# Optimization experiments

Hardware: AMD Instinct MI355X
Metric: run time of the kernel (lower is better)

Reference implementation:

```python
import jax, jax.numpy as jnp
import numpy as np

B, CIN, H, W = 32, 512, 64, 64
HID, A, C = 256, 9, 20
M = 65536


def setup_inputs() -> dict:
    key = jax.random.key(0)
    k = jax.random.split(key, 7)
    N = B * A * H * W
    features = jax.random.normal(k[0], (B, CIN, H, W), jnp.float32)
    W1 = jax.random.normal(k[1], (HID, CIN), jnp.float32) * 0.02
    b1 = jnp.zeros((HID,), jnp.float32)
    W2 = jax.random.normal(k[2], (5 * A + C, HID), jnp.float32) * 0.02
    b2 = jnp.zeros((5 * A + C,), jnp.float32)
    pos_anchor_idx = jax.random.randint(k[3], (M,), 0, N, jnp.int64 if jax.config.read('jax_enable_x64') else jnp.int32)
    neg_anchor_idx = jax.random.randint(k[4], (M,), 0, N, jnp.int64 if jax.config.read('jax_enable_x64') else jnp.int32)
    return {"features": features, "W1": W1, "b1": b1, "W2": W2, "b2": b2,
            "pos_anchor_idx": pos_anchor_idx, "neg_anchor_idx": neg_anchor_idx}


def reference(features, W1, b1, W2, b2, pos_anchor_idx, neg_anchor_idx):
    Bb, Cin, Hh, Ww = features.shape
    # 1x1 convs are channel GEMMs
    h = jnp.einsum('bchw,oc->bohw', features, W1) + b1[None, :, None, None]
    h = jax.nn.leaky_relu(h, 0.01)  # Dropout2d identity at inference
    out = jnp.einsum('bchw,oc->bohw', h, W2) + b2[None, :, None, None]
    class_scores = out[:, 5 * A:, :, :]                      # (B, C, H, W)
    anchor = out[:, :5 * A, :, :].reshape(Bb, A, 5, Hh, Ww)   # (B, A, 5, H, W)
    conf = jax.nn.sigmoid(anchor[:, :, 0:1])                  # (B, A, 1, H, W)
    off = anchor[:, :, 1:]                                    # (B, A, 4, H, W)
    off = jnp.concatenate([jax.nn.sigmoid(off[:, :, :2]) - 0.5, off[:, :, 2:]], axis=2)
    # extraction: flat layout is b*A*H*W + a*H*W + h*W + w (permute 0,1,3,4,2)
    off_flat = off.transpose(0, 1, 3, 4, 2).reshape(-1, 4)
    conf_flat = conf.transpose(0, 1, 3, 4, 2).reshape(-1, 1)
    offsets = off_flat[pos_anchor_idx]                        # (M, 4)
    conf_out = jnp.concatenate([conf_flat[pos_anchor_idx], conf_flat[neg_anchor_idx]], axis=0)  # (2M, 1)
    # class scores: expand over A is a pure broadcast, so index by (b, spatial) directly
    b_idx = pos_anchor_idx // (A * Hh * Ww)
    sp = pos_anchor_idx % (Hh * Ww)
    cls_flat = class_scores.transpose(0, 2, 3, 1).reshape(Bb * Hh * Ww, -1)
    class_out = cls_flat[b_idx * (Hh * Ww) + sp]              # (M, C)
    return conf_out, offsets, class_out
```

## Files before the change

### kernel.cpp

```cpp
#include <hip/hip_runtime.h>
#include <hip/hip_bf16.h>

typedef __attribute__((ext_vector_type(8)))  __bf16 bf16x8;
typedef __attribute__((ext_vector_type(4)))  __bf16 bf16x4;
typedef __attribute__((ext_vector_type(16))) float  f32x16;
typedef __attribute__((ext_vector_type(4)))  float  f32x4;

#define B_    32
#define CIN   512
#define HID   256
#define HW    4096
#define NA    9
#define NCH   65
#define NPADC 96
#define BN    128
#define M_    65536
#define NTOT  (B_*NA*HW)


static __device__ __forceinline__ float sigf(float v) {
    return 1.f / (1.f + __expf(-v));
}

__global__ void prep_weights(const float* __restrict__ W1, const float* __restrict__ W2,
                             unsigned short* __restrict__ W1bt, unsigned short* __restrict__ W2p) {
    int i = blockIdx.x * 256 + threadIdx.x;
    if (i < 16*256*32) {
        int kt = i >> 13, o = (i >> 5) & 255, kk = i & 31;
        __bf16 h = (__bf16)W1[o*CIN + kt*32 + kk];
        W1bt[i] = __builtin_bit_cast(unsigned short, h);
    } else {
        int j = i - 16*256*32;
        if (j < NPADC*HID) {
            int o = j >> 8, c = j & 255;
            float v = (o < NCH) ? W2[o*HID + c] : 0.f;
            __bf16 h = (__bf16)v;
            W2p[j] = __builtin_bit_cast(unsigned short, h);
        }
    }
}

__launch_bounds__(256, 2)
__global__ void fused_mlp(const float* __restrict__ feat,
                          const float* __restrict__ b1,
                          const float* __restrict__ b2,
                          const unsigned short* __restrict__ W1bt,
                          const unsigned short* __restrict__ W2p,
                          float* __restrict__ conf_d,
                          unsigned short* __restrict__ off_w,
                          unsigned short* __restrict__ cls_w) {
    __shared__ __align__(16) unsigned char smem[65536];
    unsigned short* As = (unsigned short*)smem;
    unsigned short* Bs = (unsigned short*)(smem + 20480);

    const int tid  = threadIdx.x;
    const int w    = tid >> 6;
    const int lane = tid & 63;
    const int lr   = lane & 31;
    const int lh   = lane >> 5;
    const int bidx = blockIdx.x >> 5;
    const int hw0  = (blockIdx.x & 31) * BN;

    const float* fb = feat + (size_t)bidx * CIN * HW + hw0;

    const int sA  = tid;
    const int sB  = tid & 127;
    const int kgB = tid >> 7;

    f32x16 acc[2][4];
#pragma unroll
    for (int m = 0; m < 2; ++m)
#pragma unroll
        for (int n = 0; n < 4; ++n) acc[m][n] = (f32x16)0.f;

    bf16x8 pa[4];
    float  pb[16];

    auto loadA = [&](int kt) {
        const bf16x8* p = (const bf16x8*)(W1bt + kt*8192 + sA*32);
#pragma unroll
        for (int i = 0; i < 4; ++i) pa[i] = p[i];
    };
    auto loadB = [&](int kt) {
#pragma unroll
        for (int q = 0; q < 2; ++q) {
            int kg = kgB + 2*q;
            const float* src = fb + (size_t)(kt*32 + kg*8) * HW + sB;
#pragma unroll
            for (int j = 0; j < 8; ++j) pb[q*8 + j] = src[(size_t)j * HW];
        }
    };
    auto storeAB = [&]() {
#pragma unroll
        for (int i = 0; i < 4; ++i) *(bf16x8*)(As + sA*40 + i*8) = pa[i];
#pragma unroll
        for (int q = 0; q < 2; ++q) {
            int kg = kgB + 2*q;
            bf16x8 v8;
#pragma unroll
            for (int j = 0; j < 8; ++j) v8[j] = (__bf16)pb[q*8 + j];
            *(bf16x8*)(Bs + sB*40 + kg*8) = v8;
        }
    };

    loadA(0); loadB(0);
    for (int kt = 0; kt < 16; ++kt) {
        storeAB();
        __syncthreads();
        if (kt < 15) { loadA(kt + 1); loadB(kt + 1); }
#pragma unroll
        for (int kk = 0; kk < 2; ++kk) {
            bf16x8 a0 = *(const bf16x8*)(As + (64*w      + lr)*40 + kk*16 + lh*8);
            bf16x8 a1 = *(const bf16x8*)(As + (64*w + 32 + lr)*40 + kk*16 + lh*8);
#pragma unroll
            for (int n = 0; n < 4; ++n) {
                bf16x8 bv = *(const bf16x8*)(Bs + (32*n + lr)*40 + kk*16 + lh*8);
                acc[0][n] = __builtin_amdgcn_mfma_f32_32x32x16_bf16(a0, bv, acc[0][n], 0, 0, 0);
                acc[1][n] = __builtin_amdgcn_mfma_f32_32x32x16_bf16(a1, bv, acc[1][n], 0, 0, 0);
            }
        }
        __syncthreads();
    }

#pragma unroll
    for (int m = 0; m < 2; ++m)
#pragma unroll
        for (int n = 0; n < 4; ++n) {
            int col = 32*n + lr;
            unsigned cswz = (unsigned)((col & 7) << 4);
#pragma unroll
            for (int g = 0; g < 4; ++g) {
                int rbase = 64*w + 32*m + 8*g + 4*lh;
                f32x4 b1v = *(const f32x4*)(b1 + rbase);
                bf16x4 pk;
#pragma unroll
                for (int r = 0; r < 4; ++r) {
                    float v = acc[m][n][4*g + r] + b1v[r];
                    v = v > 0.f ? v : 0.01f * v;
                    pk[r] = (__bf16)v;
                }
                unsigned addr = (unsigned)(col*512 + rbase*2) ^ cswz;
                *(bf16x4*)(smem + addr) = pk;
            }
        }
    __syncthreads();

    f32x16 acc2[3];
#pragma unroll
    for (int m = 0; m < 3; ++m) acc2[m] = (f32x16)0.f;
    const int col2 = 32*w + lr;
    const unsigned cswz2 = (unsigned)((col2 & 7) << 4);
    for (int kt2 = 0; kt2 < 8; ++kt2) {
#pragma unroll
        for (int kk = 0; kk < 2; ++kk) {
            int k0 = kt2*32 + kk*16 + lh*8;
            bf16x8 bv = *(const bf16x8*)(smem + ((unsigned)(col2*512 + k0*2) ^ cswz2));
#pragma unroll
            for (int m = 0; m < 3; ++m) {
                bf16x8 av = *(const bf16x8*)(W2p + (32*m + lr)*256 + k0);
                acc2[m] = __builtin_amdgcn_mfma_f32_32x32x16_bf16(av, bv, acc2[m], 0, 0, 0);
            }
        }
    }

    __syncthreads();
    float* so = (float*)smem;
#pragma unroll
    for (int m = 0; m < 3; ++m)
#pragma unroll
        for (int g = 0; g < 4; ++g) {
            int rbase = 32*m + 8*g + 4*lh;
            if (rbase <= 64) {
#pragma unroll
                for (int r = 0; r < 4; ++r) {
                    int row = rbase + r;
                    if (row < NCH) so[row*128 + col2] = acc2[m][4*g + r] + b2[row];
                }
            }
        }
    __syncthreads();

    {
        const int p   = tid & 127;
        const int phw = hw0 + p;
        const int b9  = bidx * NA;
        if (tid < 128) {
#pragma unroll
            for (int a = 0; a < 9; ++a) {
                float v0 = so[(5*a+0)*128 + p];
                float v1 = so[(5*a+1)*128 + p];
                float v2 = so[(5*a+2)*128 + p];
                float v3 = so[(5*a+3)*128 + p];
                float v4 = so[(5*a+4)*128 + p];
                int abase = ((b9 + a) << 12) + phw;
                conf_d[abase] = sigf(v0);
                bf16x4 o;
                o[0] = (__bf16)(sigf(v1) - 0.5f);
                o[1] = (__bf16)(sigf(v2) - 0.5f);
                o[2] = (__bf16)v3;
                o[3] = (__bf16)v4;
                *(bf16x4*)(off_w + ((size_t)abase << 2)) = o;
            }
        } else {
            unsigned short* dst = cls_w + ((size_t)((bidx << 12) + phw) << 5);
#pragma unroll
            for (int q = 0; q < 4; ++q) {
                bf16x8 v;
#pragma unroll
                for (int r = 0; r < 8; ++r) {
                    int c = q*8 + r;
                    v[r] = (c < 20) ? (__bf16)so[(45 + c)*128 + p] : (__bf16)0.f;
                }
                *(bf16x8*)(dst + q*8) = v;
            }
        }
    }
}

__global__ void gather_all(const int* __restrict__ pos, const int* __restrict__ neg,
                           const float* __restrict__ conf_d,
                           const unsigned short* __restrict__ off_w,
                           const unsigned short* __restrict__ cls_w,
                           float* __restrict__ out) {
    int t = blockIdx.x * 256 + threadIdx.x;
    if (t < 2*M_) {
        int idx = (t < M_) ? pos[t] : neg[t - M_];
        out[t] = conf_d[idx];
    } else if (t < 3*M_) {
        int i = t - 2*M_;
        int p = pos[i];
        bf16x4 o = *(const bf16x4*)(off_w + ((size_t)p << 2));
        f32x4 f;
        f[0] = (float)o[0]; f[1] = (float)o[1];
        f[2] = (float)o[2]; f[3] = (float)o[3];
        *(f32x4*)(out + 2*(size_t)M_ + 4*(size_t)i) = f;
    } else {
        int i = t - 3*M_;
        int p = pos[i];
        int hw = p & 4095;
        int b  = (p >> 12) / 9;
        const unsigned short* src = cls_w + ((size_t)((b << 12) + hw) << 5);
        float* dst = out + 6*(size_t)M_ + 20*(size_t)i;
        bf16x8 v0 = *(const bf16x8*)(src);
        bf16x8 v1 = *(const bf16x8*)(src + 8);
        bf16x4 v2 = *(const bf16x4*)(src + 16);
        f32x4 f;
        f[0] = (float)v0[0]; f[1] = (float)v0[1]; f[2] = (float)v0[2]; f[3] = (float)v0[3];
        *(f32x4*)(dst) = f;
        f[0] = (float)v0[4]; f[1] = (float)v0[5]; f[2] = (float)v0[6]; f[3] = (float)v0[7];
        *(f32x4*)(dst + 4) = f;
        f[0] = (float)v1[0]; f[1] = (float)v1[1]; f[2] = (float)v1[2]; f[3] = (float)v1[3];
        *(f32x4*)(dst + 8) = f;
        f[0] = (float)v1[4]; f[1] = (float)v1[5]; f[2] = (float)v1[6]; f[3] = (float)v1[7];
        *(f32x4*)(dst + 12) = f;
        f[0] = (float)v2[0]; f[1] = (float)v2[1]; f[2] = (float)v2[2]; f[3] = (float)v2[3];
        *(f32x4*)(dst + 16) = f;
    }
}

extern "C" void kernel_launch(void* const* d_in, const int* in_sizes, int n_in,
                              void* d_out, int out_size, void* d_ws, size_t ws_size,
                              hipStream_t stream) {
    const float* feat = (const float*)d_in[0];
    const float* W1   = (const float*)d_in[1];
    const float* b1   = (const float*)d_in[2];
    const float* W2   = (const float*)d_in[3];
    const float* b2   = (const float*)d_in[4];
    const int*   pos  = (const int*)d_in[5];
    const int*   neg  = (const int*)d_in[6];
    float* out = (float*)d_out;

    char* ws = (char*)d_ws;
    unsigned short* W1bt = (unsigned short*)ws;
    unsigned short* W2p  = (unsigned short*)(ws + 262144);
    float*          conf_d = (float*)(ws + 311296);
    unsigned short* off_w  = (unsigned short*)(ws + 5029888);
    unsigned short* cls_w  = (unsigned short*)(ws + 14467072);

    prep_weights<<<608, 256, 0, stream>>>(W1, W2, W1bt, W2p);
    fused_mlp<<<1024, 256, 0, stream>>>(feat, b1, b2, W1bt, W2p, conf_d, off_w, cls_w);
    gather_all<<<1024, 256, 0, stream>>>(pos, neg, conf_d, off_w, cls_w, out);
}
```

Measured before the change: 96.05 us.

## Double-buffer feature tiles in LDS and load W1 fragments straight to registers

The first GEMM's K-loop now prefetches feature tiles two iterations ahead into a two-stage register buffer. It keeps two LDS buffers for B, so only one barrier per iteration is needed instead of two. The W1 A-fragments are read directly from global memory into MFMA operand registers, skipping the LDS staging for A. This is meant to hide global load latency behind MFMA work and cut LDS traffic, at the cost of more registers, which could lower occupancy or cause spills under launch_bounds(256,2).

```diff
diff --git a/kernel.cpp b/kernel.cpp
--- a/kernel.cpp
+++ b/kernel.cpp
@@ -50,8 +50,6 @@
                           unsigned short* __restrict__ off_w,
                           unsigned short* __restrict__ cls_w) {
     __shared__ __align__(16) unsigned char smem[65536];
-    unsigned short* As = (unsigned short*)smem;
-    unsigned short* Bs = (unsigned short*)(smem + 20480);
 
     const int tid  = threadIdx.x;
     const int w    = tid >> 6;
@@ -63,7 +61,6 @@
 
     const float* fb = feat + (size_t)bidx * CIN * HW + hw0;
 
-    const int sA  = tid;
     const int sB  = tid & 127;
     const int kgB = tid >> 7;
 
@@ -73,52 +70,57 @@
 #pragma unroll
         for (int n = 0; n < 4; ++n) acc[m][n] = (f32x16)0.f;
 
-    bf16x8 pa[4];
-    float  pb[16];
-
-    auto loadA = [&](int kt) {
-        const bf16x8* p = (const bf16x8*)(W1bt + kt*8192 + sA*32);
-#pragma unroll
-        for (int i = 0; i < 4; ++i) pa[i] = p[i];
+    float  pb[2][16];
+    bf16x8 aw[2][4];
+
+    auto issueB = [&](int kt, int s) {
+#pragma unroll
+        for (int q = 0; q < 2; ++q) {
+            const float* src = fb + (size_t)(kt*32 + (kgB + 2*q)*8) * HW + sB;
+#pragma unroll
+            for (int j = 0; j < 8; ++j) pb[s][q*8 + j] = src[(size_t)j * HW];
+        }
     };
-    auto loadB = [&](int kt) {
+    auto issueA = [&](int kt, int s) {
+#pragma unroll
+        for (int kk = 0; kk < 2; ++kk)
+#pragma unroll
+            for (int m = 0; m < 2; ++m)
+                aw[s][kk*2 + m] = *(const bf16x8*)(W1bt + kt*8192 + (64*w + 32*m + lr)*32 + kk*16 + lh*8);
+    };
+    auto storeB = [&](int s) {
+        unsigned short* Bst = (unsigned short*)(smem + s*10240);
 #pragma unroll
         for (int q = 0; q < 2; ++q) {
-            int kg = kgB + 2*q;
-            const float* src = fb + (size_t)(kt*32 + kg*8) * HW + sB;
-#pragma unroll
-            for (int j = 0; j < 8; ++j) pb[q*8 + j] = src[(size_t)j * HW];
+            bf16x8 v8;
+#pragma unroll
+            for (int j = 0; j < 8; ++j) v8[j] = (__bf16)pb[s][q*8 + j];
+            *(bf16x8*)(Bst + sB*40 + (kgB + 2*q)*8) = v8;
         }
     };
-    auto storeAB = [&]() {
-#pragma unroll
-        for (int i = 0; i < 4; ++i) *(bf16x8*)(As + sA*40 + i*8) = pa[i];
-#pragma unroll
-        for (int q = 0; q < 2; ++q) {
-            int kg = kgB + 2*q;
-            bf16x8 v8;
-#pragma unroll
-            for (int j = 0; j < 8; ++j) v8[j] = (__bf16)pb[q*8 + j];
-            *(bf16x8*)(Bs + sB*40 + kg*8) = v8;
-        }
-    };
-
-    loadA(0); loadB(0);
+
+    issueB(0, 0); issueB(1, 1); issueA(0, 0);
+    storeB(0);
+    __syncthreads();
+
+#pragma unroll
     for (int kt = 0; kt < 16; ++kt) {
-        storeAB();
-        __syncthreads();
-        if (kt < 15) { loadA(kt + 1); loadB(kt + 1); }
+        const int cur = kt & 1, nxt = cur ^ 1;
+        if (kt + 2 < 16) issueB(kt + 2, cur);
+        if (kt + 1 < 16) issueA(kt + 1, nxt);
+        const unsigned short* Bst = (const unsigned short*)(smem + cur*10240);
 #pragma unroll
         for (int kk = 0; kk < 2; ++kk) {
-            bf16x8 a0 = *(const bf16x8*)(As + (64*w      + lr)*40 + kk*16 + lh*8);
-            bf16x8 a1 = *(const bf16x8*)(As + (64*w + 32 + lr)*40 + kk*16 + lh*8);
+            bf16x8 a0 = aw[cur][kk*2 + 0];
+            bf16x8 a1 = aw[cur][kk*2 + 1];
 #pragma unroll
             for (int n = 0; n < 4; ++n) {
-                bf16x8 bv = *(const bf16x8*)(Bs + (32*n + lr)*40 + kk*16 + lh*8);
+                bf16x8 bv = *(const bf16x8*)(Bst + (32*n + lr)*40 + kk*16 + lh*8);
                 acc[0][n] = __builtin_amdgcn_mfma_f32_32x32x16_bf16(a0, bv, acc[0][n], 0, 0, 0);
                 acc[1][n] = __builtin_amdgcn_mfma_f32_32x32x16_bf16(a1, bv, acc[1][n], 0, 0, 0);
             }
         }
+        if (kt + 1 < 16) storeB(nxt);
         __syncthreads();
     }
 
```

Result: slower. 99.70 us (+3.8%).
